# Optimization experiments

Hardware: AMD Instinct MI355X
Metric: run time of the kernel (lower is better)

The kernel has to match this reference:

```python
import jax, jax.numpy as jnp
import numpy as np

D_MODEL, N_EXPERTS, N_VIEWS, N_TOKENS = 256, 16, 3, 8192

def setup_inputs() -> dict:
    key = jax.random.key(0)
    ks = jax.random.split(key, 10)
    s = 0.05
    return {
        "v0": jax.random.normal(ks[0], (N_TOKENS, D_MODEL), jnp.float32),
        "v1": jax.random.normal(ks[1], (N_TOKENS, D_MODEL), jnp.float32),
        "v2": jax.random.normal(ks[2], (N_TOKENS, D_MODEL), jnp.float32),
        "router_w": jax.random.normal(ks[3], (N_VIEWS, N_EXPERTS, D_MODEL), jnp.float32) * s,
        "expert_keys": jax.random.normal(ks[4], (N_EXPERTS, D_MODEL), jnp.float32) * s,
        "W1": jax.random.normal(ks[5], (N_EXPERTS, D_MODEL, 4 * D_MODEL), jnp.float32) * s,
        "b1": jax.random.normal(ks[6], (N_EXPERTS, 4 * D_MODEL), jnp.float32) * s,
        "W2": jax.random.normal(ks[7], (N_EXPERTS, 4 * D_MODEL, D_MODEL), jnp.float32) * s,
        "b2": jax.random.normal(ks[8], (N_EXPERTS, D_MODEL), jnp.float32) * s,
        "top_k": 4,
    }

def _laplace_gate(v, rw, expert_keys, top_k):
    # -||v - key||^2 expanded: -(|v|^2 + |k|^2 - 2 v.k)   -> [N, E]
    sq = (jnp.sum(v * v, -1, keepdims=True)
          + jnp.sum(expert_keys * expert_keys, -1)[None, :]
          - 2.0 * (v @ expert_keys.T))
    logits = -sq + v @ rw.T                      # router(h), no bias
    topv, topi = jax.lax.top_k(logits, top_k)    # [N, K]
    gate = jax.nn.softmax(topv, axis=-1)         # exp(topv - logsumexp(topv))
    return gate, topi

def reference(v0, v1, v2, router_w, expert_keys, W1, b1, W2, b2, top_k):
    views = [v0, v1, v2]
    E = expert_keys.shape[0]
    N = v0.shape[0]
    fused = jnp.zeros_like(v0)
    rows = jnp.arange(N)[:, None]
    for i, v in enumerate(views):
        gate, idx = _laplace_gate(v, router_w[i], expert_keys, top_k)
        # scatter top-k gates into a dense [N, E] combine matrix
        dense_gate = jnp.zeros((N, E), v.dtype).at[rows, idx].add(gate)
        out = jnp.zeros_like(v)
        for e in range(E):  # fixed small expert loop; each token combined via its gate
            h = jax.nn.gelu(v @ W1[e] + b1[e], approximate=False)
            out = out + dense_gate[:, e:e + 1] * (h @ W2[e] + b2[e])
        fused = fused + out
    return fused
```

## Files before the change

kernel.cpp:

```cpp
#include <hip/hip_runtime.h>
#include <math.h>

#define D_MODEL 256
#define N_EXP   16
#define N_VIEWS 3
#define N_TOK   8192
#define TOPK    4
#define HDIM    1024
#define CH      64
#define NCH     16
#define NSUB    32
#define ROWS    64
#define TI_MAX  40
#define NGROUP  48
#define GCAP    8192
#define REC_ELTS 32768

typedef short s16x8 __attribute__((ext_vector_type(8)));
typedef float f32x4 __attribute__((ext_vector_type(4)));

__device__ __forceinline__ unsigned short f2bf(float x) {
    union { float f; unsigned u; } a; a.f = x;
    unsigned r = a.u + 0x7FFFu + ((a.u >> 16) & 1u);
    return (unsigned short)(r >> 16);
}

__device__ __forceinline__ void dma16(const unsigned short* gp, unsigned short* lp) {
    __builtin_amdgcn_global_load_lds(
        (const __attribute__((address_space(1))) unsigned int*)gp,
        (__attribute__((address_space(3))) unsigned int*)lp, 16, 0, 0);
}

__device__ __forceinline__ void dma_sub(const unsigned short* wrec0, int sc,
                                        unsigned short* ldst, int wave, int lane) {
    const unsigned short* g = wrec0 + (size_t)(sc >> 1) * REC_ELTS
                                    + (size_t)((wave * 4 + (sc & 1) * 2) * 512);
    dma16(g + lane * 8,       ldst + wave * 1024);
    dma16(g + 512 + lane * 8, ldst + wave * 1024 + 512);
}

#define T1_STRIDE 65
#define T2_STRIDE 257

__global__ __launch_bounds__(256) void wfrag_kernel(
    const float* __restrict__ W1, const float* __restrict__ W2,
    unsigned short* __restrict__ Wf)
{
    __shared__ __align__(16) char smem[256 * T1_STRIDE * 4];

    int bid = blockIdx.x;
    int tid = threadIdx.x;
    int c = bid & 15, e = (bid >> 4) & 15, z = bid >> 8;
    unsigned short* dst = Wf + (size_t)(e * NCH + c) * REC_ELTS;
    if (z == 0) {
        float* T1 = (float*)smem;
        const float* src = W1 + (size_t)e * 256 * 1024 + c * 64;
        #pragma unroll
        for (int p = 0; p < 16; p++) {
            int k = p * 16 + (tid >> 4), c4 = (tid & 15) * 4;
            float4 v = *(const float4*)(src + (size_t)k * 1024 + c4);
            T1[k * T1_STRIDE + c4]     = v.x;
            T1[k * T1_STRIDE + c4 + 1] = v.y;
            T1[k * T1_STRIDE + c4 + 2] = v.z;
            T1[k * T1_STRIDE + c4 + 3] = v.w;
        }
        __syncthreads();
        #pragma unroll
        for (int i = 0; i < 8; i++) {
            int idx = tid + i * 256;
            int lane = idx & 63, nt = (idx >> 6) & 3, ks = idx >> 8;
            int nl = nt * 16 + (lane & 15);
            int kbase = ks * 32 + (lane >> 4) * 8;
            s16x8 o;
            #pragma unroll
            for (int j = 0; j < 8; j++) o[j] = (short)f2bf(T1[(kbase + j) * T1_STRIDE + nl]);
            *(s16x8*)(dst + (size_t)idx * 8) = o;
        }
    } else {
        float* T2 = (float*)smem;
        const float* src = W2 + ((size_t)e * 1024 + c * 64) * 256;
        #pragma unroll
        for (int p = 0; p < 16; p++) {
            int k2l = p * 4 + (tid >> 6), c4 = (tid & 63) * 4;
            float4 v = *(const float4*)(src + (size_t)k2l * 256 + c4);
            T2[k2l * T2_STRIDE + c4]     = v.x;
            T2[k2l * T2_STRIDE + c4 + 1] = v.y;
            T2[k2l * T2_STRIDE + c4 + 2] = v.z;
            T2[k2l * T2_STRIDE + c4 + 3] = v.w;
        }
        __syncthreads();
        dst += 16384;
        #pragma unroll
        for (int i = 0; i < 8; i++) {
            int idx = tid + i * 256;
            int lane = idx & 63, ntile = (idx >> 6) & 15, ks2 = idx >> 10;
            int n = ntile * 16 + (lane & 15);
            int kbase = ks2 * 32 + (lane >> 4) * 8;
            s16x8 o;
            #pragma unroll
            for (int j = 0; j < 8; j++) o[j] = (short)f2bf(T2[(kbase + j) * T2_STRIDE + n]);
            *(s16x8*)(dst + (size_t)idx * 8) = o;
        }
    }
}

__global__ __launch_bounds__(256) void route_kernel(
    const float* __restrict__ v0, const float* __restrict__ v1, const float* __restrict__ v2,
    const float* __restrict__ rw, const float* __restrict__ keys,
    unsigned short* __restrict__ Xbf,
    int* __restrict__ counts, int* __restrict__ rowTok, float* __restrict__ rowGate)
{
    __shared__ __align__(16) float XsT[256 * 64];
    __shared__ __align__(16) float cwS[16 * 256];
    __shared__ float logitS[64 * 17];
    __shared__ float knS[16];
    __shared__ int   lcnt[16], lbase[16], fpos[16];
    __shared__ int   eIdx[256];
    __shared__ float gV[256];

    int rb = blockIdx.x;
    int view = rb >> 7, xb = rb & 127;
    const float* src = view == 0 ? v0 : (view == 1 ? v1 : v2);
    int tid = threadIdx.x;

    for (int i = tid; i < N_EXP * D_MODEL; i += 256)
        cwS[i] = rw[view * N_EXP * D_MODEL + i] + 2.0f * keys[i];
    if (tid < N_EXP) {
        const float4* kp = (const float4*)(keys + tid * D_MODEL);
        float s = 0.f;
        for (int d = 0; d < 64; d++) { float4 k = kp[d]; s += k.x*k.x + k.y*k.y + k.z*k.z + k.w*k.w; }
        knS[tid] = s; lcnt[tid] = 0; fpos[tid] = 0;
    }
    {
        int t = tid >> 2, q = tid & 3;
        int token = xb * 64 + t;
        const float4* vp = (const float4*)(src + (size_t)token * D_MODEL + q * 64);
        ushort4* xo = (ushort4*)(Xbf + ((size_t)view * N_TOK + token) * D_MODEL + q * 64);
        #pragma unroll
        for (int i = 0; i < 16; i++) {
            float4 v = vp[i];
            ushort4 h; h.x = f2bf(v.x); h.y = f2bf(v.y); h.z = f2bf(v.z); h.w = f2bf(v.w);
            xo[i] = h;
            int d = q * 64 + i * 4;
            XsT[(d + 0) * 64 + t] = v.x;
            XsT[(d + 1) * 64 + t] = v.y;
            XsT[(d + 2) * 64 + t] = v.z;
            XsT[(d + 3) * 64 + t] = v.w;
        }
    }
    __syncthreads();

    int wave = tid >> 6, lane = tid & 63;

    {
        const float* xcol = &XsT[lane];
        const float* c0 = &cwS[(wave * 4 + 0) * D_MODEL];
        const float* c1 = &cwS[(wave * 4 + 1) * D_MODEL];
        const float* c2 = &cwS[(wave * 4 + 2) * D_MODEL];
        const float* c3 = &cwS[(wave * 4 + 3) * D_MODEL];
        float a0 = 0.f, a1 = 0.f, a2 = 0.f, a3 = 0.f;
        #pragma unroll 4
        for (int d4 = 0; d4 < 64; d4++) {
            float x0 = xcol[(d4 * 4 + 0) * 64];
            float x1 = xcol[(d4 * 4 + 1) * 64];
            float x2 = xcol[(d4 * 4 + 2) * 64];
            float x3 = xcol[(d4 * 4 + 3) * 64];
            float4 w0 = *(const float4*)(c0 + d4 * 4);
            float4 w1 = *(const float4*)(c1 + d4 * 4);
            float4 w2 = *(const float4*)(c2 + d4 * 4);
            float4 w3 = *(const float4*)(c3 + d4 * 4);
            a0 += x0 * w0.x + x1 * w0.y + x2 * w0.z + x3 * w0.w;
            a1 += x0 * w1.x + x1 * w1.y + x2 * w1.z + x3 * w1.w;
            a2 += x0 * w2.x + x1 * w2.y + x2 * w2.z + x3 * w2.w;
            a3 += x0 * w3.x + x1 * w3.y + x2 * w3.z + x3 * w3.w;
        }
        logitS[lane * 17 + wave * 4 + 0] = a0 - knS[wave * 4 + 0];
        logitS[lane * 17 + wave * 4 + 1] = a1 - knS[wave * 4 + 1];
        logitS[lane * 17 + wave * 4 + 2] = a2 - knS[wave * 4 + 2];
        logitS[lane * 17 + wave * 4 + 3] = a3 - knS[wave * 4 + 3];
    }
    __syncthreads();

    if (tid < 64) {
        int tl = tid;
        float lg[N_EXP];
        #pragma unroll
        for (int e = 0; e < N_EXP; e++) lg[e] = logitS[tl * 17 + e];
        int idxs[TOPK]; float vals[TOPK];
        #pragma unroll
        for (int k = 0; k < TOPK; k++) {
            float best = -1e30f; int bi = 0;
            #pragma unroll
            for (int e = 0; e < N_EXP; e++)
                if (lg[e] > best) { best = lg[e]; bi = e; }
            idxs[k] = bi; vals[k] = best;
            #pragma unroll
            for (int e = 0; e < N_EXP; e++)
                lg[e] = (e == bi) ? -1e30f : lg[e];
        }
        float m = vals[0], s = 0.f, ex[TOPK];
        #pragma unroll
        for (int k = 0; k < TOPK; k++) { ex[k] = __expf(vals[k] - m); s += ex[k]; }
        float inv = 1.0f / s;
        #pragma unroll
        for (int k = 0; k < TOPK; k++) {
            eIdx[tl * 4 + k] = idxs[k];
            gV[tl * 4 + k]   = ex[k] * inv;
            atomicAdd(&lcnt[idxs[k]], 1);
        }
    }
    __syncthreads();
    if (tid < N_EXP)
        lbase[tid] = lcnt[tid] ? atomicAdd(&counts[view * N_EXP + tid], lcnt[tid]) : 0;
    __syncthreads();
    {
        int e  = eIdx[tid];
        float gv = gV[tid];
        int pos = atomicAdd(&fpos[e], 1);
        int dst = (view * N_EXP + e) * GCAP + lbase[e] + pos;
        rowTok[dst]  = xb * 64 + (tid >> 2);
        rowGate[dst] = gv;
    }
}

__global__ __launch_bounds__(512, 4) void ffn_kernel(
    const unsigned short* __restrict__ Xbf, const unsigned short* __restrict__ Wf,
    const float* __restrict__ b1, const float* __restrict__ b2,
    const int* __restrict__ counts, const int* __restrict__ rowTok,
    const float* __restrict__ rowGate, float* __restrict__ out)
{
    __shared__ __align__(16) unsigned short W1buf[4][8192];
    __shared__ __align__(16) unsigned short Hc[2][2048];

    int s = blockIdx.x;
    int xcd = s & 7, k = s >> 3;
    int j = k % 6, ti = k / 6;
    int e = 2 * xcd + (j & 1), view = j >> 1;
    int g = view * N_EXP + e;
    int L = counts[g];
    int r0 = ti * ROWS;
    if (r0 >= L) return;
    int base = g * GCAP;

    int tid = threadIdx.x;
    int wave = tid >> 6, lane = tid & 63, lmod = lane & 15, quad = lane >> 4;

    const unsigned short* wchunk = Wf + (size_t)e * NCH * REC_ELTS;

    int mt1 = wave & 3, nh = wave >> 2;
    int ms  = wave & 1, ns = wave >> 1;

    s16x8 areg[8];
    {
        int gr = r0 + mt1 * 16 + lmod;
        int token = (gr < L) ? rowTok[base + gr] : 0;
        const unsigned short* xp = Xbf + ((size_t)view * N_TOK + token) * D_MODEL;
        #pragma unroll
        for (int ks = 0; ks < 8; ks++)
            areg[ks] = *(const s16x8*)(xp + ks * 32 + quad * 8);
    }
    float bbCur = b1[e * HDIM + nh * 16 + lmod];

    f32x4 acc2[2][4];
    #pragma unroll
    for (int i = 0; i < 2; i++)
        #pragma unroll
        for (int jj = 0; jj < 4; jj++) acc2[i][jj] = (f32x4){0.f, 0.f, 0.f, 0.f};

    __builtin_amdgcn_sched_barrier(0);
    dma_sub(wchunk, 0, &W1buf[0][0], wave, lane);
    __builtin_amdgcn_sched_barrier(0);
    dma_sub(wchunk, 1, &W1buf[1][0], wave, lane);
    __builtin_amdgcn_sched_barrier(0);
    dma_sub(wchunk, 2, &W1buf[2][0], wave, lane);
    __builtin_amdgcn_sched_barrier(0);
    asm volatile("s_waitcnt vmcnt(4)" ::: "memory");
    __builtin_amdgcn_sched_barrier(0);
    __builtin_amdgcn_s_barrier();
    __builtin_amdgcn_sched_barrier(0);

    s16x8 w2r[4] = {};

    #pragma unroll 1
    for (int cc = 0; cc < NSUB; cc++) {
        int bn = (cc + 1 < NSUB) ? cc + 1 : NSUB - 1;
        float bbNext = b1[e * HDIM + bn * 32 + nh * 16 + lmod];

        const unsigned short* w1s = &W1buf[cc & 3][0];
        f32x4 a1a = (f32x4){0.f, 0.f, 0.f, 0.f};
        f32x4 a1b = (f32x4){0.f, 0.f, 0.f, 0.f};
        __builtin_amdgcn_s_setprio(1);
        #pragma unroll
        for (int ks = 0; ks < 8; ks += 2) {
            s16x8 bw0 = *(const s16x8*)(w1s + ks * 1024 + nh * 512 + lane * 8);
            s16x8 bw1 = *(const s16x8*)(w1s + (ks + 1) * 1024 + nh * 512 + lane * 8);
            a1a = __builtin_amdgcn_mfma_f32_16x16x32_bf16(areg[ks],     bw0, a1a, 0, 0, 0);
            a1b = __builtin_amdgcn_mfma_f32_16x16x32_bf16(areg[ks + 1], bw1, a1b, 0, 0, 0);
        }
        __builtin_amdgcn_s_setprio(0);

        {
            unsigned short* hd = &Hc[cc & 1][0];
            int bo = mt1 * 512 + (nh * 2 + (lmod >> 3)) * 128 + quad * 32 + (lmod & 7);
            #pragma unroll
            for (int r = 0; r < 4; r++) {
                float h = a1a[r] + a1b[r] + bbCur;
                float u = h * (0.7978845608f + 0.0356774081f * h * h);
                float ex2 = __expf(2.f * u);
                float tn = 1.f - 2.f * __builtin_amdgcn_rcpf(1.f + ex2);
                hd[bo + r * 8] = f2bf(0.5f * h * (1.f + tn));
            }
        }

        if (cc > 0) {
            const unsigned short* hs = &Hc[(cc - 1) & 1][0];
            s16x8 afr[2];
            #pragma unroll
            for (int mt = 0; mt < 2; mt++)
                afr[mt] = *(const s16x8*)(hs + ((ms * 2 + mt) * 64 + lane) * 8);
            __builtin_amdgcn_s_setprio(1);
            #pragma unroll
            for (int nt = 0; nt < 4; nt++)
                #pragma unroll
                for (int mt = 0; mt < 2; mt++)
                    acc2[mt][nt] = __builtin_amdgcn_mfma_f32_16x16x32_bf16(
                        afr[mt], w2r[nt], acc2[mt][nt], 0, 0, 0);
            __builtin_amdgcn_s_setprio(0);
        }

        {
            const unsigned short* w2p = wchunk + (size_t)(cc >> 1) * REC_ELTS + 16384
                                        + (size_t)(((cc & 1) * 16 + ns * 4) * 512);
            #pragma unroll
            for (int nt = 0; nt < 4; nt++)
                w2r[nt] = *(const s16x8*)(w2p + nt * 512 + lane * 8);
        }

        __builtin_amdgcn_sched_barrier(0);
        if (cc + 3 < NSUB)
            dma_sub(wchunk, cc + 3, &W1buf[(cc + 3) & 3][0], wave, lane);
        __builtin_amdgcn_sched_barrier(0);

        bbCur = bbNext;

        asm volatile("s_waitcnt vmcnt(9) lgkmcnt(0)" ::: "memory");
        __builtin_amdgcn_sched_barrier(0);
        __builtin_amdgcn_s_barrier();
        __builtin_amdgcn_sched_barrier(0);
    }

    asm volatile("s_waitcnt vmcnt(0)" ::: "memory");

    {
        const unsigned short* hs = &Hc[(NSUB - 1) & 1][0];
        s16x8 afr[2];
        #pragma unroll
        for (int mt = 0; mt < 2; mt++)
            afr[mt] = *(const s16x8*)(hs + ((ms * 2 + mt) * 64 + lane) * 8);
        #pragma unroll
        for (int nt = 0; nt < 4; nt++)
            #pragma unroll
            for (int mt = 0; mt < 2; mt++)
                acc2[mt][nt] = __builtin_amdgcn_mfma_f32_16x16x32_bf16(
                    afr[mt], w2r[nt], acc2[mt][nt], 0, 0, 0);
    }

    int   tokR[2][4];
    float gateR[2][4];
    #pragma unroll
    for (int mt = 0; mt < 2; mt++)
        #pragma unroll
        for (int r = 0; r < 4; r++) {
            int gr = r0 + (ms * 2 + mt) * 16 + quad * 4 + r;
            bool ok = gr < L;
            tokR[mt][r]  = ok ? rowTok[base + gr] : -1;
            gateR[mt][r] = ok ? rowGate[base + gr] : 0.f;
        }
    #pragma unroll
    for (int nt = 0; nt < 4; nt++) {
        int col = (ns * 4 + nt) * 16 + lmod;
        float b2v = b2[e * D_MODEL + col];
        #pragma unroll
        for (int mt = 0; mt < 2; mt++) {
            #pragma unroll
            for (int r = 0; r < 4; r++) {
                if (tokR[mt][r] >= 0) {
                    atomicAdd(&out[(size_t)tokR[mt][r] * D_MODEL + col],
                              gateR[mt][r] * (acc2[mt][nt][r] + b2v));
                }
            }
        }
    }
}

extern "C" void kernel_launch(void* const* d_in, const int* in_sizes, int n_in,
                              void* d_out, int out_size, void* d_ws, size_t ws_size,
                              hipStream_t stream)
{
    const float* v0   = (const float*)d_in[0];
    const float* v1   = (const float*)d_in[1];
    const float* v2   = (const float*)d_in[2];
    const float* rw   = (const float*)d_in[3];
    const float* keys = (const float*)d_in[4];
    const float* W1   = (const float*)d_in[5];
    const float* b1   = (const float*)d_in[6];
    const float* W2   = (const float*)d_in[7];
    const float* b2   = (const float*)d_in[8];
    float* out = (float*)d_out;

    char* p = (char*)d_ws;
    unsigned short* Xbf = (unsigned short*)p; p += (size_t)N_VIEWS * N_TOK * D_MODEL * 2;
    unsigned short* Wf  = (unsigned short*)p; p += (size_t)N_EXP * NCH * REC_ELTS * 2;
    int*   counts = (int*)p;   p += 256;
    int*   rowTok = (int*)p;   p += (size_t)NGROUP * GCAP * 4;
    float* rowGate= (float*)p; p += (size_t)NGROUP * GCAP * 4;

    hipMemsetAsync(counts, 0, NGROUP * sizeof(int), stream);
    hipMemsetAsync(out, 0, (size_t)out_size * sizeof(float), stream);

    wfrag_kernel<<<512, 256, 0, stream>>>(W1, W2, Wf);
    route_kernel<<<384, 256, 0, stream>>>(v0, v1, v2, rw, keys, Xbf,
                                          counts, rowTok, rowGate);
    ffn_kernel<<<8 * 6 * TI_MAX, 512, 0, stream>>>(Xbf, Wf, b1, b2, counts,
                                                   rowTok, rowGate, out);
}
```

Measured before the change: 327.9 us.

## Merge weight-fragment prep and routing kernels into one interleaved launch

Combines the weight bf16 fragment conversion and the routing/gating kernel into a single prep kernel with 896 blocks. Blocks are interleaved 4:3 between weight-conversion and routing work so the two independent jobs run concurrently. The routing path now stages the token tile in two halves, cutting XsT shared memory from 64KB to 32KB so both roles fit a common ~65KB shared allocation. This removes one launch and the serialization between the two kernels, at the cost of an extra barrier per half and a larger shared footprint for the weight blocks.

```diff
diff --git a/kernel.cpp b/kernel.cpp
--- a/kernel.cpp
+++ b/kernel.cpp
@@ -42,86 +42,89 @@
 #define T1_STRIDE 65
 #define T2_STRIDE 257
 
-__global__ __launch_bounds__(256) void wfrag_kernel(
+__global__ __launch_bounds__(256) void prep_kernel(
+    const float* __restrict__ v0, const float* __restrict__ v1, const float* __restrict__ v2,
+    const float* __restrict__ rw, const float* __restrict__ keys,
     const float* __restrict__ W1, const float* __restrict__ W2,
-    unsigned short* __restrict__ Wf)
+    unsigned short* __restrict__ Wf, unsigned short* __restrict__ Xbf,
+    int* __restrict__ counts, int* __restrict__ rowTok, float* __restrict__ rowGate)
 {
-    __shared__ __align__(16) char smem[256 * T1_STRIDE * 4];
+    __shared__ __align__(16) char smem[66560];
 
     int bid = blockIdx.x;
     int tid = threadIdx.x;
-    int c = bid & 15, e = (bid >> 4) & 15, z = bid >> 8;
-    unsigned short* dst = Wf + (size_t)(e * NCH + c) * REC_ELTS;
-    if (z == 0) {
-        float* T1 = (float*)smem;
-        const float* src = W1 + (size_t)e * 256 * 1024 + c * 64;
-        #pragma unroll
-        for (int p = 0; p < 16; p++) {
-            int k = p * 16 + (tid >> 4), c4 = (tid & 15) * 4;
-            float4 v = *(const float4*)(src + (size_t)k * 1024 + c4);
-            T1[k * T1_STRIDE + c4]     = v.x;
-            T1[k * T1_STRIDE + c4 + 1] = v.y;
-            T1[k * T1_STRIDE + c4 + 2] = v.z;
-            T1[k * T1_STRIDE + c4 + 3] = v.w;
-        }
-        __syncthreads();
-        #pragma unroll
-        for (int i = 0; i < 8; i++) {
-            int idx = tid + i * 256;
-            int lane = idx & 63, nt = (idx >> 6) & 3, ks = idx >> 8;
-            int nl = nt * 16 + (lane & 15);
-            int kbase = ks * 32 + (lane >> 4) * 8;
-            s16x8 o;
-            #pragma unroll
-            for (int j = 0; j < 8; j++) o[j] = (short)f2bf(T1[(kbase + j) * T1_STRIDE + nl]);
-            *(s16x8*)(dst + (size_t)idx * 8) = o;
-        }
-    } else {
-        float* T2 = (float*)smem;
-        const float* src = W2 + ((size_t)e * 1024 + c * 64) * 256;
-        #pragma unroll
-        for (int p = 0; p < 16; p++) {
-            int k2l = p * 4 + (tid >> 6), c4 = (tid & 63) * 4;
-            float4 v = *(const float4*)(src + (size_t)k2l * 256 + c4);
-            T2[k2l * T2_STRIDE + c4]     = v.x;
-            T2[k2l * T2_STRIDE + c4 + 1] = v.y;
-            T2[k2l * T2_STRIDE + c4 + 2] = v.z;
-            T2[k2l * T2_STRIDE + c4 + 3] = v.w;
-        }
-        __syncthreads();
-        dst += 16384;
-        #pragma unroll
-        for (int i = 0; i < 8; i++) {
-            int idx = tid + i * 256;
-            int lane = idx & 63, ntile = (idx >> 6) & 15, ks2 = idx >> 10;
-            int n = ntile * 16 + (lane & 15);
-            int kbase = ks2 * 32 + (lane >> 4) * 8;
-            s16x8 o;
-            #pragma unroll
-            for (int j = 0; j < 8; j++) o[j] = (short)f2bf(T2[(kbase + j) * T2_STRIDE + n]);
-            *(s16x8*)(dst + (size_t)idx * 8) = o;
-        }
-    }
-}
-
-__global__ __launch_bounds__(256) void route_kernel(
-    const float* __restrict__ v0, const float* __restrict__ v1, const float* __restrict__ v2,
-    const float* __restrict__ rw, const float* __restrict__ keys,
-    unsigned short* __restrict__ Xbf,
-    int* __restrict__ counts, int* __restrict__ rowTok, float* __restrict__ rowGate)
-{
-    __shared__ __align__(16) float XsT[256 * 64];
-    __shared__ __align__(16) float cwS[16 * 256];
-    __shared__ float logitS[64 * 17];
-    __shared__ float knS[16];
-    __shared__ int   lcnt[16], lbase[16], fpos[16];
-    __shared__ int   eIdx[256];
-    __shared__ float gV[256];
-
-    int rb = blockIdx.x;
+    int sept = bid / 7, r7 = bid % 7;
+
+    if (r7 < 4) {
+        int wb = sept * 4 + r7;
+        int c = wb & 15, e = (wb >> 4) & 15, z = wb >> 8;
+        unsigned short* dst = Wf + (size_t)(e * NCH + c) * REC_ELTS;
+        if (z == 0) {
+            float* T1 = (float*)smem;
+            const float* src = W1 + (size_t)e * 256 * 1024 + c * 64;
+            #pragma unroll
+            for (int p = 0; p < 16; p++) {
+                int k = p * 16 + (tid >> 4), c4 = (tid & 15) * 4;
+                float4 v = *(const float4*)(src + (size_t)k * 1024 + c4);
+                T1[k * T1_STRIDE + c4]     = v.x;
+                T1[k * T1_STRIDE + c4 + 1] = v.y;
+                T1[k * T1_STRIDE + c4 + 2] = v.z;
+                T1[k * T1_STRIDE + c4 + 3] = v.w;
+            }
+            __syncthreads();
+            #pragma unroll
+            for (int i = 0; i < 8; i++) {
+                int idx = tid + i * 256;
+                int lane = idx & 63, nt = (idx >> 6) & 3, ks = idx >> 8;
+                int nl = nt * 16 + (lane & 15);
+                int kbase = ks * 32 + (lane >> 4) * 8;
+                s16x8 o;
+                #pragma unroll
+                for (int j = 0; j < 8; j++) o[j] = (short)f2bf(T1[(kbase + j) * T1_STRIDE + nl]);
+                *(s16x8*)(dst + (size_t)idx * 8) = o;
+            }
+        } else {
+            float* T2 = (float*)smem;
+            const float* src = W2 + ((size_t)e * 1024 + c * 64) * 256;
+            #pragma unroll
+            for (int p = 0; p < 16; p++) {
+                int k2l = p * 4 + (tid >> 6), c4 = (tid & 63) * 4;
+                float4 v = *(const float4*)(src + (size_t)k2l * 256 + c4);
+                T2[k2l * T2_STRIDE + c4]     = v.x;
+                T2[k2l * T2_STRIDE + c4 + 1] = v.y;
+                T2[k2l * T2_STRIDE + c4 + 2] = v.z;
+                T2[k2l * T2_STRIDE + c4 + 3] = v.w;
+            }
+            __syncthreads();
+            dst += 16384;
+            #pragma unroll
+            for (int i = 0; i < 8; i++) {
+                int idx = tid + i * 256;
+                int lane = idx & 63, ntile = (idx >> 6) & 15, ks2 = idx >> 10;
+                int n = ntile * 16 + (lane & 15);
+                int kbase = ks2 * 32 + (lane >> 4) * 8;
+                s16x8 o;
+                #pragma unroll
+                for (int j = 0; j < 8; j++) o[j] = (short)f2bf(T2[(kbase + j) * T2_STRIDE + n]);
+                *(s16x8*)(dst + (size_t)idx * 8) = o;
+            }
+        }
+        return;
+    }
+
+    int rb = sept * 3 + (r7 - 4);
+    float* XsT    = (float*)smem;
+    float* cwS    = (float*)(smem + 32768);
+    float* logitS = (float*)(smem + 49152);
+    float* knS    = (float*)(smem + 53504);
+    int*   lcnt   = (int*)(smem + 53568);
+    int*   lbase  = (int*)(smem + 53632);
+    int*   fpos   = (int*)(smem + 53696);
+    int*   eIdx   = (int*)(smem + 53760);
+    float* gV     = (float*)(smem + 54784);
+
     int view = rb >> 7, xb = rb & 127;
     const float* src = view == 0 ? v0 : (view == 1 ? v1 : v2);
-    int tid = threadIdx.x;
 
     for (int i = tid; i < N_EXP * D_MODEL; i += 256)
         cwS[i] = rw[view * N_EXP * D_MODEL + i] + 2.0f * keys[i];
@@ -131,54 +134,58 @@
         for (int d = 0; d < 64; d++) { float4 k = kp[d]; s += k.x*k.x + k.y*k.y + k.z*k.z + k.w*k.w; }
         knS[tid] = s; lcnt[tid] = 0; fpos[tid] = 0;
     }
-    {
-        int t = tid >> 2, q = tid & 3;
-        int token = xb * 64 + t;
-        const float4* vp = (const float4*)(src + (size_t)token * D_MODEL + q * 64);
-        ushort4* xo = (ushort4*)(Xbf + ((size_t)view * N_TOK + token) * D_MODEL + q * 64);
-        #pragma unroll
-        for (int i = 0; i < 16; i++) {
-            float4 v = vp[i];
-            ushort4 h; h.x = f2bf(v.x); h.y = f2bf(v.y); h.z = f2bf(v.z); h.w = f2bf(v.w);
-            xo[i] = h;
-            int d = q * 64 + i * 4;
-            XsT[(d + 0) * 64 + t] = v.x;
-            XsT[(d + 1) * 64 + t] = v.y;
-            XsT[(d + 2) * 64 + t] = v.z;
-            XsT[(d + 3) * 64 + t] = v.w;
-        }
-    }
-    __syncthreads();
 
     int wave = tid >> 6, lane = tid & 63;
-
-    {
-        const float* xcol = &XsT[lane];
-        const float* c0 = &cwS[(wave * 4 + 0) * D_MODEL];
-        const float* c1 = &cwS[(wave * 4 + 1) * D_MODEL];
-        const float* c2 = &cwS[(wave * 4 + 2) * D_MODEL];
-        const float* c3 = &cwS[(wave * 4 + 3) * D_MODEL];
-        float a0 = 0.f, a1 = 0.f, a2 = 0.f, a3 = 0.f;
-        #pragma unroll 4
-        for (int d4 = 0; d4 < 64; d4++) {
-            float x0 = xcol[(d4 * 4 + 0) * 64];
-            float x1 = xcol[(d4 * 4 + 1) * 64];
-            float x2 = xcol[(d4 * 4 + 2) * 64];
-            float x3 = xcol[(d4 * 4 + 3) * 64];
-            float4 w0 = *(const float4*)(c0 + d4 * 4);
-            float4 w1 = *(const float4*)(c1 + d4 * 4);
-            float4 w2 = *(const float4*)(c2 + d4 * 4);
-            float4 w3 = *(const float4*)(c3 + d4 * 4);
-            a0 += x0 * w0.x + x1 * w0.y + x2 * w0.z + x3 * w0.w;
-            a1 += x0 * w1.x + x1 * w1.y + x2 * w1.z + x3 * w1.w;
-            a2 += x0 * w2.x + x1 * w2.y + x2 * w2.z + x3 * w2.w;
-            a3 += x0 * w3.x + x1 * w3.y + x2 * w3.z + x3 * w3.w;
-        }
-        logitS[lane * 17 + wave * 4 + 0] = a0 - knS[wave * 4 + 0];
-        logitS[lane * 17 + wave * 4 + 1] = a1 - knS[wave * 4 + 1];
-        logitS[lane * 17 + wave * 4 + 2] = a2 - knS[wave * 4 + 2];
-        logitS[lane * 17 + wave * 4 + 3] = a3 - knS[wave * 4 + 3];
-    }
+    float a0 = 0.f, a1 = 0.f, a2 = 0.f, a3 = 0.f;
+
+    #pragma unroll 1
+    for (int p = 0; p < 2; p++) {
+        {
+            int t = tid >> 2, q = tid & 3;
+            int token = xb * 64 + t;
+            const float4* vp = (const float4*)(src + (size_t)token * D_MODEL + p * 128 + q * 32);
+            ushort4* xo = (ushort4*)(Xbf + ((size_t)view * N_TOK + token) * D_MODEL + p * 128 + q * 32);
+            #pragma unroll
+            for (int i = 0; i < 8; i++) {
+                float4 v = vp[i];
+                ushort4 h; h.x = f2bf(v.x); h.y = f2bf(v.y); h.z = f2bf(v.z); h.w = f2bf(v.w);
+                xo[i] = h;
+                int d = q * 32 + i * 4;
+                XsT[(d + 0) * 64 + t] = v.x;
+                XsT[(d + 1) * 64 + t] = v.y;
+                XsT[(d + 2) * 64 + t] = v.z;
+                XsT[(d + 3) * 64 + t] = v.w;
+            }
+        }
+        __syncthreads();
+        {
+            const float* xcol = &XsT[lane];
+            const float* c0 = &cwS[(wave * 4 + 0) * D_MODEL + p * 128];
+            const float* c1 = &cwS[(wave * 4 + 1) * D_MODEL + p * 128];
+            const float* c2 = &cwS[(wave * 4 + 2) * D_MODEL + p * 128];
+            const float* c3 = &cwS[(wave * 4 + 3) * D_MODEL + p * 128];
+            #pragma unroll 4
+            for (int d4 = 0; d4 < 32; d4++) {
+                float x0 = xcol[(d4 * 4 + 0) * 64];
+                float x1 = xcol[(d4 * 4 + 1) * 64];
+                float x2 = xcol[(d4 * 4 + 2) * 64];
+                float x3 = xcol[(d4 * 4 + 3) * 64];
+                float4 w0 = *(const float4*)(c0 + d4 * 4);
+                float4 w1 = *(const float4*)(c1 + d4 * 4);
+                float4 w2 = *(const float4*)(c2 + d4 * 4);
+                float4 w3 = *(const float4*)(c3 + d4 * 4);
+                a0 += x0 * w0.x + x1 * w0.y + x2 * w0.z + x3 * w0.w;
+                a1 += x0 * w1.x + x1 * w1.y + x2 * w1.z + x3 * w1.w;
+                a2 += x0 * w2.x + x1 * w2.y + x2 * w2.z + x3 * w2.w;
+                a3 += x0 * w3.x + x1 * w3.y + x2 * w3.z + x3 * w3.w;
+            }
+        }
+        __syncthreads();
+    }
+    logitS[lane * 17 + wave * 4 + 0] = a0 - knS[wave * 4 + 0];
+    logitS[lane * 17 + wave * 4 + 1] = a1 - knS[wave * 4 + 1];
+    logitS[lane * 17 + wave * 4 + 2] = a2 - knS[wave * 4 + 2];
+    logitS[lane * 17 + wave * 4 + 3] = a3 - knS[wave * 4 + 3];
     __syncthreads();
 
     if (tid < 64) {
@@ -418,9 +425,8 @@
     hipMemsetAsync(counts, 0, NGROUP * sizeof(int), stream);
     hipMemsetAsync(out, 0, (size_t)out_size * sizeof(float), stream);
 
-    wfrag_kernel<<<512, 256, 0, stream>>>(W1, W2, Wf);
-    route_kernel<<<384, 256, 0, stream>>>(v0, v1, v2, rw, keys, Xbf,
-                                          counts, rowTok, rowGate);
+    prep_kernel<<<896, 256, 0, stream>>>(v0, v1, v2, rw, keys, W1, W2,
+                                         Wf, Xbf, counts, rowTok, rowGate);
     ffn_kernel<<<8 * 6 * TI_MAX, 512, 0, stream>>>(Xbf, Wf, b1, b2, counts,
                                                    rowTok, rowGate, out);
 }
```

New measurement: 320.9 us. 1.02x faster.
